# Performance work log

Measured on AMD Instinct MI355X. Metric: run time of the kernel, lower is better.

The kernel has to match this reference:

```python
import jax, jax.numpy as jnp
import numpy as np

B, C, H, W = 16, 3, 224, 224
P = 16
DIM = 256
NL = 8
DS = 16          # d_state (mamba default)
DCONV = 4
NCLS = 1000
DI = 2 * DIM     # expand * dim
DTR = -(-DIM // 16)  # dt_rank = ceil(dim/16)
NPATCH = (H // P) * (W // P)
SEQ = NPATCH + 1


def _ln(x, g, b, eps=1e-5):
    mu = x.mean(-1, keepdims=True)
    var = ((x - mu) ** 2).mean(-1, keepdims=True)
    return (x - mu) * jax.lax.rsqrt(var + eps) * g + b


def setup_inputs() -> dict:
    key = jax.random.key(0)
    ks = jax.random.split(key, 12)
    pd = C * P * P
    s = 0.02
    return dict(
        img=jax.random.normal(ks[0], (B, C, H, W), jnp.float32),
        pe_ln1_g=jnp.ones((pd,), jnp.float32), pe_ln1_b=jnp.zeros((pd,), jnp.float32),
        pe_w=jax.random.normal(ks[1], (pd, DIM), jnp.float32) * s,
        pe_b=jnp.zeros((DIM,), jnp.float32),
        pe_ln2_g=jnp.ones((DIM,), jnp.float32), pe_ln2_b=jnp.zeros((DIM,), jnp.float32),
        pos_emb=jax.random.normal(ks[2], (1, SEQ, DIM), jnp.float32) * s,
        cls_tok=jax.random.normal(ks[3], (1, 1, DIM), jnp.float32) * s,
        ln_w=jnp.ones((NL, DIM), jnp.float32), ln_b=jnp.zeros((NL, DIM), jnp.float32),
        in_w=jax.random.normal(ks[4], (NL, DIM, 2 * DI), jnp.float32) * s,
        conv_w=jax.random.normal(ks[5], (NL, DI, DCONV), jnp.float32) * s,
        conv_b=jnp.zeros((NL, DI), jnp.float32),
        xproj_w=jax.random.normal(ks[6], (NL, DI, DTR + 2 * DS), jnp.float32) * s,
        dtproj_w=jax.random.normal(ks[7], (NL, DTR, DI), jnp.float32) * s,
        dtproj_b=jax.random.uniform(ks[8], (NL, DI), jnp.float32, -4.0, -2.0),
        A_log=jnp.log(jnp.broadcast_to(jnp.arange(1, DS + 1, dtype=jnp.float32), (NL, DI, DS))) + jnp.zeros((NL, DI, DS), jnp.float32),
        Dp=jnp.ones((NL, DI), jnp.float32),
        out_w=jax.random.normal(ks[9], (NL, DI, DIM), jnp.float32) * s,
        normf_w=jnp.ones((DIM,), jnp.float32), normf_b=jnp.zeros((DIM,), jnp.float32),
        head_w=jax.random.normal(ks[10], (DIM, NCLS), jnp.float32) * s,
        head_b=jnp.zeros((NCLS,), jnp.float32),
    )


def _mamba(x, in_w, conv_w, conv_b, xproj_w, dtproj_w, dtproj_b, A_log, Dp, out_w):
    b, L, _ = x.shape
    xz = x @ in_w                       # (b, L, 2*DI)
    xm, z = jnp.split(xz, 2, axis=-1)
    # causal depthwise conv1d (torch pads both sides then slices -> left-pad d_conv-1)
    xc = jnp.pad(xm.transpose(0, 2, 1), ((0, 0), (0, 0), (DCONV - 1, 0)))
    xc = jax.lax.conv_general_dilated(
        xc, conv_w[:, None, :], (1,), 'VALID',
        dimension_numbers=('NCH', 'OIH', 'NCH'), feature_group_count=DI)
    u = jax.nn.silu(xc + conv_b[None, :, None]).transpose(0, 2, 1)  # (b, L, DI)
    dbc = u @ xproj_w                   # (b, L, DTR+2*DS)
    dt, Bm, Cm = jnp.split(dbc, [DTR, DTR + DS], axis=-1)
    dt = jax.nn.softplus(dt @ dtproj_w + dtproj_b)  # (b, L, DI)
    A = -jnp.exp(A_log)                 # (DI, DS)

    def step(h, inp):
        dt_t, B_t, C_t, u_t = inp       # (b,DI), (b,DS), (b,DS), (b,DI)
        dA = jnp.exp(dt_t[:, :, None] * A)                 # (b, DI, DS)
        h = dA * h + (dt_t * u_t)[:, :, None] * B_t[:, None, :]
        y = jnp.einsum('bdn,bn->bd', h, C_t)
        return h, y

    h0 = jnp.zeros((b, DI, DS), x.dtype)
    xs = (dt.transpose(1, 0, 2), Bm.transpose(1, 0, 2),
          Cm.transpose(1, 0, 2), u.transpose(1, 0, 2))
    _, ys = jax.lax.scan(step, h0, xs)
    y = ys.transpose(1, 0, 2) + u * Dp  # (b, L, DI)
    y = y * jax.nn.silu(z)
    return y @ out_w                    # (b, L, DIM)


def reference(img, pe_ln1_g, pe_ln1_b, pe_w, pe_b, pe_ln2_g, pe_ln2_b, pos_emb,
              cls_tok, ln_w, ln_b, in_w, conv_w, conv_b, xproj_w, dtproj_w,
              dtproj_b, A_log, Dp, out_w, normf_w, normf_b, head_w, head_b):
    b = img.shape[0]
    h, w = H // P, W // P
    # 'b c (h p1) (w p2) -> b (h w) (p1 p2 c)'
    x = img.reshape(b, C, h, P, w, P).transpose(0, 2, 4, 3, 5, 1).reshape(b, h * w, P * P * C)
    x = _ln(x, pe_ln1_g, pe_ln1_b)
    x = x @ pe_w + pe_b
    x = _ln(x, pe_ln2_g, pe_ln2_b)
    x = jnp.concatenate([jnp.broadcast_to(cls_tok, (b, 1, DIM)), x], axis=1)
    x = x + pos_emb[:, :x.shape[1]]
    residual = None
    for i in range(NL):
        residual = x if residual is None else x + residual
        xn = _ln(residual, ln_w[i], ln_b[i])
        x = _mamba(xn, in_w[i], conv_w[i], conv_b[i], xproj_w[i],
                   dtproj_w[i], dtproj_b[i], A_log[i], Dp[i], out_w[i])
    residual = x + residual
    x = _ln(residual, normf_w, normf_b)
    x = x[:, 0]                          # pool == 'cls'
    return x @ head_w + head_b
```

## Files before the change

### kernel.cpp

```cpp
#include <hip/hip_runtime.h>
#include <math.h>

#define NB   16
#define SEQL 197
#define TB   (NB*SEQL)
#define DIMM 256
#define DI   512
#define DS   16
#define NL   8

typedef __bf16 bf16x8 __attribute__((ext_vector_type(8)));
typedef __bf16 bf16x4 __attribute__((ext_vector_type(4)));
typedef float floatx4 __attribute__((ext_vector_type(4)));

__device__ __forceinline__ void block_reduce_2(float& s1, float& s2, float* red, int tid){
  #pragma unroll
  for (int off = 32; off > 0; off >>= 1){
    s1 += __shfl_down(s1, off, 64);
    s2 += __shfl_down(s2, off, 64);
  }
  __syncthreads();
  if ((tid & 63) == 0){ red[(tid>>6)*2] = s1; red[(tid>>6)*2+1] = s2; }
  __syncthreads();
  s1 = red[0] + red[2] + red[4] + red[6];
  s2 = red[1] + red[3] + red[5] + red[7];
}

__global__ __launch_bounds__(256) void prep_weights(
    const float* __restrict__ in_w, const float* __restrict__ out_w,
    const float* __restrict__ pe_w, const float* __restrict__ xproj,
    __bf16* __restrict__ wt_in, __bf16* __restrict__ wt_out,
    __bf16* __restrict__ wt_pe, __bf16* __restrict__ wt_xp)
{
  __shared__ float t[32][33];
  int bid = blockIdx.x;
  const float* src; __bf16* dst;
  int K, Nin, n0, k0;
  if (bid < 2048){
    int z = bid >> 8, tt = bid & 255;
    K = 256; Nin = 1024; n0 = (tt & 31)*32; k0 = (tt >> 5)*32;
    src = in_w  + (size_t)z*K*Nin;
    dst = wt_in + (size_t)z*K*Nin;
  } else if (bid < 3072){
    int t2 = bid - 2048; int z = t2 >> 7, tt = t2 & 127;
    K = 512; Nin = 256; n0 = (tt & 7)*32; k0 = (tt >> 3)*32;
    src = out_w  + (size_t)z*K*Nin;
    dst = wt_out + (size_t)z*K*Nin;
  } else if (bid < 3264){
    int tt = bid - 3072;
    K = 768; Nin = 256; n0 = (tt & 7)*32; k0 = (tt >> 3)*32;
    src = pe_w; dst = wt_pe;
  } else {
    int t2 = bid - 3264; int z = t2 >> 5, tt = t2 & 31;
    K = 512; Nin = 48; n0 = (tt & 1)*32; k0 = (tt >> 1)*32;
    src = xproj + (size_t)z*K*Nin;
    dst = wt_xp + (size_t)z*64*K;
  }
  int tx = threadIdx.x & 31, ty = threadIdx.x >> 5;
  #pragma unroll
  for (int j = 0; j < 4; j++){
    int n = n0 + tx;
    t[ty + j*8][tx] = (n < Nin) ? src[(size_t)(k0 + ty + j*8)*Nin + n] : 0.f;
  }
  __syncthreads();
  #pragma unroll
  for (int j = 0; j < 4; j++)
    dst[(size_t)(n0 + ty + j*8)*K + k0 + tx] = (__bf16)t[tx][ty + j*8];
}

template<int BM, int BN, int KS>
__global__ __launch_bounds__(256) void gemm_bf16(
    const __bf16* __restrict__ A, const __bf16* __restrict__ Wt,
    const float* __restrict__ bias, float* __restrict__ C, int M, int N, int K)
{
  constexpr int BK  = 32;
  constexpr int LDA = BK + 8;
  constexpr int TMW = BM/32;
  constexpr int TNW = BN/32;
  __shared__ __bf16 As[BM][LDA];
  __shared__ __bf16 Bs[BN][LDA];

  int tid  = threadIdx.x;
  int lane = tid & 63, w = tid >> 6;
  int wm = w >> 1, wn = w & 1;
  int l15 = lane & 15, quad = lane >> 4;
  int nt = blockIdx.x / KS, ks = blockIdx.x % KS;
  int bm = blockIdx.y * BM, bn = nt * BN;
  int kbeg = ks * (K / KS), kend = kbeg + (K / KS);

  floatx4 acc[TMW][TNW] = {};

  for (int k0 = kbeg; k0 < kend; k0 += BK){
    #pragma unroll
    for (int i = 0; i < BM/64; i++){
      int c = tid + i*256;
      int row = c >> 2, kc = c & 3;
      int m = bm + row;
      uint4 v = make_uint4(0,0,0,0);
      if (m < M) v = ((const uint4*)(A + (size_t)m*K + k0))[kc];
      *(uint4*)&As[row][kc*8] = v;
    }
    #pragma unroll
    for (int i = 0; i < BN/64; i++){
      int c = tid + i*256;
      int row = c >> 2, kc = c & 3;
      int n = bn + row;
      uint4 v = ((const uint4*)(Wt + (size_t)n*K + k0))[kc];
      *(uint4*)&Bs[row][kc*8] = v;
    }
    __syncthreads();
    bf16x8 af[TMW], bf[TNW];
    #pragma unroll
    for (int mi = 0; mi < TMW; mi++)
      af[mi] = *(const bf16x8*)&As[wm*(BM/2) + mi*16 + l15][quad*8];
    #pragma unroll
    for (int ni = 0; ni < TNW; ni++)
      bf[ni] = *(const bf16x8*)&Bs[wn*(BN/2) + ni*16 + l15][quad*8];
    #pragma unroll
    for (int mi = 0; mi < TMW; mi++)
      #pragma unroll
      for (int ni = 0; ni < TNW; ni++)
        acc[mi][ni] = __builtin_amdgcn_mfma_f32_16x16x32_bf16(af[mi], bf[ni], acc[mi][ni], 0, 0, 0);
    __syncthreads();
  }
  #pragma unroll
  for (int mi = 0; mi < TMW; mi++){
    #pragma unroll
    for (int ni = 0; ni < TNW; ni++){
      int col = bn + wn*(BN/2) + ni*16 + l15;
      float bv = (KS == 1 && bias) ? bias[col] : 0.f;
      #pragma unroll
      for (int r = 0; r < 4; r++){
        int row = bm + wm*(BM/2) + mi*16 + quad*4 + r;
        if (row < M){
          if (KS == 1) C[(size_t)row*N + col] = acc[mi][ni][r] + bv;
          else         atomicAdd(&C[(size_t)row*N + col], acc[mi][ni][r]);
        }
      }
    }
  }
}

template<int DO_LN>
__global__ __launch_bounds__(512) void gemm_out_fused(
    const __bf16* __restrict__ A, const __bf16* __restrict__ Wt,
    float* __restrict__ resid, __bf16* __restrict__ xn_bf,
    const float* __restrict__ g, const float* __restrict__ bta)
{
  constexpr int BK = 64, LDA = BK + 8;
  __shared__ alignas(16) char smem[(16 + 256) * LDA * sizeof(__bf16)];
  __bf16 (*As)[LDA] = (__bf16(*)[LDA])smem;
  __bf16 (*Bs)[LDA] = (__bf16(*)[LDA])(smem + 16*LDA*sizeof(__bf16));
  float  (*sy)[264] = (float(*)[264])smem;

  int tid = threadIdx.x, lane = tid & 63, w = tid >> 6;
  int l15 = lane & 15, quad = lane >> 4;
  int bm = blockIdx.x * 16;

  floatx4 acc[2] = {};
  for (int k0 = 0; k0 < 512; k0 += BK){
    if (tid < 128){
      int row = tid >> 3, kc = tid & 7;
      *(uint4*)&As[row][kc*8] = ((const uint4*)(A + (size_t)(bm+row)*512 + k0))[kc];
    }
    #pragma unroll
    for (int i = 0; i < 4; i++){
      int c = tid + i*512;
      int row = c >> 3, kc = c & 7;
      *(uint4*)&Bs[row][kc*8] = ((const uint4*)(Wt + (size_t)row*512 + k0))[kc];
    }
    __syncthreads();
    #pragma unroll
    for (int kk = 0; kk < 2; kk++){
      bf16x8 af = *(const bf16x8*)&As[l15][kk*32 + quad*8];
      #pragma unroll
      for (int ni = 0; ni < 2; ni++){
        bf16x8 bfv = *(const bf16x8*)&Bs[w*32 + ni*16 + l15][kk*32 + quad*8];
        acc[ni] = __builtin_amdgcn_mfma_f32_16x16x32_bf16(af, bfv, acc[ni], 0, 0, 0);
      }
    }
    __syncthreads();
  }
  #pragma unroll
  for (int ni = 0; ni < 2; ni++){
    int col = w*32 + ni*16 + l15;
    #pragma unroll
    for (int r = 0; r < 4; r++)
      sy[quad*4 + r][col] = acc[ni][r];
  }
  __syncthreads();
  #pragma unroll
  for (int rr = 0; rr < 2; rr++){
    int row = w*2 + rr;
    size_t base = (size_t)(bm + row)*256 + lane*4;
    float4 y4 = *(const float4*)&sy[row][lane*4];
    float4 rv = *(const float4*)&resid[base];
    float4 v;
    v.x = y4.x + rv.x; v.y = y4.y + rv.y; v.z = y4.z + rv.z; v.w = y4.w + rv.w;
    *(float4*)&resid[base] = v;
    if (DO_LN){
      float s  = v.x + v.y + v.z + v.w;
      float s2 = v.x*v.x + v.y*v.y + v.z*v.z + v.w*v.w;
      #pragma unroll
      for (int off = 1; off < 64; off <<= 1){
        s  += __shfl_xor(s,  off, 64);
        s2 += __shfl_xor(s2, off, 64);
      }
      float mu  = s * (1.f/256.f);
      float var = s2 * (1.f/256.f) - mu*mu;
      float rrq = rsqrtf(var + 1e-5f);
      float4 gv = *(const float4*)&g[lane*4];
      float4 bv = *(const float4*)&bta[lane*4];
      bf16x4 o;
      o[0] = (__bf16)((v.x - mu)*rrq*gv.x + bv.x);
      o[1] = (__bf16)((v.y - mu)*rrq*gv.y + bv.y);
      o[2] = (__bf16)((v.z - mu)*rrq*gv.z + bv.z);
      o[3] = (__bf16)((v.w - mu)*rrq*gv.w + bv.w);
      *(bf16x4*)&xn_bf[base] = o;
    }
  }
}

__global__ __launch_bounds__(256) void patch_ln1(
    const float* __restrict__ img, const float* __restrict__ g1, const float* __restrict__ b1,
    __bf16* __restrict__ xp_bf)
{
  __shared__ float red[8];
  int blk = blockIdx.x;
  int b = blk / 196, p = blk % 196;
  int hh = p / 14, ww = p % 14;
  int tid = threadIdx.x;

  float v[3]; float s = 0.f, s2 = 0.f;
  #pragma unroll
  for (int i = 0; i < 3; i++){
    int e  = tid + i*256;
    int c  = e % 3;
    int p2 = (e/3) % 16;
    int p1 = e / 48;
    float val = img[((b*3 + c)*224 + hh*16 + p1)*224 + ww*16 + p2];
    v[i] = val; s += val; s2 += val*val;
  }
  block_reduce_2(s, s2, red, tid);
  float mu = s * (1.f/768.f);
  float var = s2 * (1.f/768.f) - mu*mu;
  float rr = rsqrtf(var + 1e-5f);
  #pragma unroll
  for (int i = 0; i < 3; i++){
    int e = tid + i*256;
    xp_bf[(size_t)blk*768 + e] = (__bf16)((v[i] - mu) * rr * g1[e] + b1[e]);
  }
}

__global__ __launch_bounds__(256) void ln2_cls_pos(
    const float* __restrict__ pemb, const float* __restrict__ g2, const float* __restrict__ b2,
    const float* __restrict__ pos, const float* __restrict__ cls,
    float* __restrict__ resid,
    const float* __restrict__ g0, const float* __restrict__ b0,
    __bf16* __restrict__ xn_bf)
{
  __shared__ float red[8];
  int blk = blockIdx.x;
  int b = blk / SEQL, l = blk % SEQL;
  int tid = threadIdx.x;
  float o;
  if (l == 0){
    o = cls[tid] + pos[tid];
  } else {
    int p = l - 1;
    float v = pemb[(size_t)(b*196 + p)*256 + tid];
    float s = v, s2 = v*v;
    block_reduce_2(s, s2, red, tid);
    float mu = s * (1.f/256.f);
    float var = s2 * (1.f/256.f) - mu*mu;
    float rr = rsqrtf(var + 1e-5f);
    o = (v - mu) * rr * g2[tid] + b2[tid] + pos[l*256 + tid];
  }
  size_t idx = (size_t)blk*256 + tid;
  resid[idx] = o;
  float s = o, s2 = o*o;
  block_reduce_2(s, s2, red, tid);
  float mu = s * (1.f/256.f);
  float var = s2 * (1.f/256.f) - mu*mu;
  float rr = rsqrtf(var + 1e-5f);
  xn_bf[idx] = (__bf16)((o - mu) * rr * g0[tid] + b0[tid]);
}

__global__ __launch_bounds__(256) void conv_silu(
    const float* __restrict__ xz, const float* __restrict__ cw, const float* __restrict__ cb,
    float* __restrict__ u, __bf16* __restrict__ u_bf, float* __restrict__ dbc)
{
  int gid = blockIdx.x*256 + threadIdx.x;
  int dq = gid & 127;
  int t = gid >> 7;
  int d = dq*4;
  int l = t % SEQL;
  const float4 z4 = make_float4(0.f,0.f,0.f,0.f);
  if (dq < 16) *(float4*)&dbc[(size_t)t*64 + d] = z4;
  float4 x0 = *(const float4*)&xz[(size_t)t*1024 + d];
  float4 x1 = (l>=1) ? *(const float4*)&xz[(size_t)(t-1)*1024 + d] : z4;
  float4 x2 = (l>=2) ? *(const float4*)&xz[(size_t)(t-2)*1024 + d] : z4;
  float4 x3 = (l>=3) ? *(const float4*)&xz[(size_t)(t-3)*1024 + d] : z4;
  float4 w0 = *(const float4*)&cw[(d+0)*4];
  float4 w1 = *(const float4*)&cw[(d+1)*4];
  float4 w2 = *(const float4*)&cw[(d+2)*4];
  float4 w3 = *(const float4*)&cw[(d+3)*4];
  float4 r = *(const float4*)&cb[d];
  r.x += x3.x*w0.x + x2.x*w0.y + x1.x*w0.z + x0.x*w0.w;
  r.y += x3.y*w1.x + x2.y*w1.y + x1.y*w1.z + x0.y*w1.w;
  r.z += x3.z*w2.x + x2.z*w2.y + x1.z*w2.z + x0.z*w2.w;
  r.w += x3.w*w3.x + x2.w*w3.y + x1.w*w3.z + x0.w*w3.w;
  r.x *= 1.f/(1.f + __expf(-r.x));
  r.y *= 1.f/(1.f + __expf(-r.y));
  r.z *= 1.f/(1.f + __expf(-r.z));
  r.w *= 1.f/(1.f + __expf(-r.w));
  *(float4*)&u[(size_t)t*512 + d] = r;
  bf16x4 o; o[0]=(__bf16)r.x; o[1]=(__bf16)r.y; o[2]=(__bf16)r.z; o[3]=(__bf16)r.w;
  *(bf16x4*)&u_bf[(size_t)t*512 + d] = o;
}

#define SCT 32
#define NCH ((SEQL + SCT - 1)/SCT)
#define NDL 8
__global__ __launch_bounds__(128) void scan_kernel(
    const float* __restrict__ u, const float* __restrict__ dbc,
    const float* __restrict__ xz, const float* __restrict__ A_log, const float* __restrict__ Dp,
    const float* __restrict__ dtw, const float* __restrict__ dtb,
    __bf16* __restrict__ yg_bf)
{
  __shared__ float s_D [16][36];
  __shared__ float s_B [16][36];
  __shared__ float s_C [16][36];
  __shared__ float s_u [NDL][36];
  __shared__ float s_z [NDL][36];
  __shared__ float s_dt[NDL][36];
  __shared__ float s_yp[SCT][NDL][20];
  __shared__ float s_dp[NDL];

  int tid = threadIdx.x;
  int n = tid & 15, dl = tid >> 4;
  int b = blockIdx.x >> 6, dg = blockIdx.x & 63;
  int d0 = dg * NDL;
  const size_t base = (size_t)b * SEQL;

  float A = -__expf(A_log[(d0+dl)*DS + n]);
  float h = 0.f;
  if (tid < NDL) s_dp[tid] = Dp[d0 + tid];
  int cch = tid & 7;
  float wc[16];
  #pragma unroll
  for (int k = 0; k < 16; k++) wc[k] = dtw[k*512 + d0 + cch];
  float dtbv = dtb[d0 + cch];

  float r_u[2], r_z[2], r_db[12];
  auto load_regs = [&](int c){
    #pragma unroll
    for (int i = 0; i < 2; i++){
      int v = tid + i*128;
      int tg = c*SCT + (v>>3); if (tg > SEQL-1) tg = SEQL-1;
      size_t t = base + tg;
      r_u[i] = u [t*512 + d0 + (v&7)];
      r_z[i] = xz[t*1024 + 512 + d0 + (v&7)];
    }
    #pragma unroll
    for (int s = 0; s < 3; s++)
      #pragma unroll
      for (int i = 0; i < 4; i++){
        int v = tid + i*128;
        int tg = c*SCT + (v>>4); if (tg > SEQL-1) tg = SEQL-1;
        r_db[s*4+i] = dbc[(base + tg)*64 + s*16 + (v&15)];
      }
  };
  auto write_DBC = [&](){
    #pragma unroll
    for (int i = 0; i < 4; i++){
      int v = tid + i*128;
      s_D[v&15][v>>4] = r_db[0+i];
      s_B[v&15][v>>4] = r_db[4+i];
      s_C[v&15][v>>4] = r_db[8+i];
    }
  };
  auto write_UZ = [&](){
    #pragma unroll
    for (int i = 0; i < 2; i++){
      int v = tid + i*128;
      s_u[v&7][v>>3] = r_u[i];
      s_z[v&7][v>>3] = r_z[i];
    }
  };
  auto compute_dt = [&](){
    #pragma unroll
    for (int i = 0; i < 2; i++){
      int tl = (tid >> 3) + i*16;
      float acc = dtbv;
      #pragma unroll
      for (int k = 0; k < 16; k++) acc += s_D[k][tl] * wc[k];
      s_dt[cch][tl] = (acc > 20.f) ? acc : log1pf(__expf(acc));
    }
  };

  load_regs(0);
  write_DBC();
  write_UZ();
  __syncthreads();
  compute_dt();
  __syncthreads();

  for (int c = 0; c < NCH; c++){
    if (c + 1 < NCH) load_regs(c+1);

    float4 dt4, u4, B4, C4;
    #pragma unroll
    for (int tl = 0; tl < SCT; tl++){
      if ((tl & 3) == 0){
        dt4 = *(const float4*)&s_dt[dl][tl];
        u4  = *(const float4*)&s_u [dl][tl];
        B4  = *(const float4*)&s_B [n][tl];
        C4  = *(const float4*)&s_C [n][tl];
      }
      float dtv = ((float*)&dt4)[tl&3];
      float uv  = ((float*)&u4 )[tl&3];
      float Bv  = ((float*)&B4 )[tl&3];
      float Cv  = ((float*)&C4 )[tl&3];
      h = __expf(dtv * A) * h + (dtv * uv) * Bv;
      s_yp[tl][dl][n] = h * Cv;
    }
    __syncthreads();

    if (c + 1 < NCH) write_DBC();

    #pragma unroll
    for (int j = 0; j < 2; j++){
      int p = tid + j*128;
      int tl = p >> 3, dr = p & 7;
      float4 a0 = *(const float4*)&s_yp[tl][dr][0];
      float4 a1 = *(const float4*)&s_yp[tl][dr][4];
      float4 a2 = *(const float4*)&s_yp[tl][dr][8];
      float4 a3 = *(const float4*)&s_yp[tl][dr][12];
      float yv = ((a0.x+a0.y)+(a0.z+a0.w)) + ((a1.x+a1.y)+(a1.z+a1.w))
               + ((a2.x+a2.y)+(a2.z+a2.w)) + ((a3.x+a3.y)+(a3.z+a3.w));
      int tg = c*SCT + tl;
      if (tg < SEQL){
        float uv = s_u[dr][tl];
        float zv = s_z[dr][tl];
        float sg = 1.f / (1.f + __expf(-zv));
        yg_bf[(base + tg)*512 + d0 + dr] = (__bf16)((yv + uv*s_dp[dr]) * zv * sg);
      }
    }
    __syncthreads();

    if (c + 1 < NCH){
      write_UZ();
      compute_dt();
      __syncthreads();
    }
  }
}

__global__ __launch_bounds__(256) void final_ln(
    const float* __restrict__ resid,
    const float* __restrict__ g, const float* __restrict__ bta, float* __restrict__ xs_g)
{
  __shared__ float red[8];
  int b = blockIdx.x, tid = threadIdx.x;
  size_t idx = (size_t)b*SEQL*256 + tid;
  float r = resid[idx];
  float s = r, s2 = r*r;
  block_reduce_2(s, s2, red, tid);
  float mu = s * (1.f/256.f);
  float var = s2 * (1.f/256.f) - mu*mu;
  float rr = rsqrtf(var + 1e-5f);
  xs_g[b*256 + tid] = (r - mu) * rr * g[tid] + bta[tid];
}

__global__ __launch_bounds__(256) void head_gemm(
    const float* __restrict__ xs_g, const float* __restrict__ head_w,
    const float* __restrict__ head_b, float* __restrict__ out)
{
  __shared__ float xs[16][256];
  int tid = threadIdx.x;
  #pragma unroll
  for (int i = 0; i < 16; i++) ((float*)xs)[tid + i*256] = xs_g[tid + i*256];
  __syncthreads();
  int nl = tid & 31, bq = tid >> 5;
  int nn = blockIdx.x*32 + nl;
  if (nn >= 1000) return;
  float acc0 = 0.f, acc1 = 0.f;
  #pragma unroll 8
  for (int k = 0; k < 256; k++){
    float w = head_w[k*1000 + nn];
    acc0 += xs[bq][k]   * w;
    acc1 += xs[bq+8][k] * w;
  }
  float hb = head_b[nn];
  out[(size_t)bq*1000 + nn]     = acc0 + hb;
  out[(size_t)(bq+8)*1000 + nn] = acc1 + hb;
}

extern "C" void kernel_launch(void* const* d_in, const int* in_sizes, int n_in,
                              void* d_out, int out_size, void* d_ws, size_t ws_size,
                              hipStream_t stream) {
  const float* img   = (const float*)d_in[0];
  const float* ln1g  = (const float*)d_in[1];
  const float* ln1b  = (const float*)d_in[2];
  const float* pe_w  = (const float*)d_in[3];
  const float* pe_b  = (const float*)d_in[4];
  const float* ln2g  = (const float*)d_in[5];
  const float* ln2b  = (const float*)d_in[6];
  const float* pos   = (const float*)d_in[7];
  const float* cls   = (const float*)d_in[8];
  const float* ln_w  = (const float*)d_in[9];
  const float* ln_b  = (const float*)d_in[10];
  const float* in_w  = (const float*)d_in[11];
  const float* conv_w= (const float*)d_in[12];
  const float* conv_b= (const float*)d_in[13];
  const float* xproj = (const float*)d_in[14];
  const float* dtw   = (const float*)d_in[15];
  const float* dtb   = (const float*)d_in[16];
  const float* A_log = (const float*)d_in[17];
  const float* Dp    = (const float*)d_in[18];
  const float* out_w = (const float*)d_in[19];
  const float* nfw   = (const float*)d_in[20];
  const float* nfb   = (const float*)d_in[21];
  const float* head_w= (const float*)d_in[22];
  const float* head_b= (const float*)d_in[23];
  float* out = (float*)d_out;

  float* ws = (float*)d_ws;
  float* resid = ws;  ws += (size_t)TB*DIMM;
  float* xz    = ws;  ws += (size_t)TB*2*DI;
  float* u     = ws;  ws += (size_t)TB*DI;
  float* dbc   = ws;  ws += (size_t)TB*64;
  float* xs_g  = ws;  ws += (size_t)NB*DIMM;
  __bf16* xn_bf = (__bf16*)ws;  ws += (size_t)TB*DIMM/2;
  __bf16* u_bf  = (__bf16*)ws;  ws += (size_t)TB*DI/2;
  __bf16* yg_bf = (__bf16*)ws;  ws += (size_t)TB*DI/2;
  __bf16* wt_in = (__bf16*)ws;  ws += (size_t)NL*1024*256/2;
  __bf16* wt_out= (__bf16*)ws;  ws += (size_t)NL*256*512/2;
  __bf16* wt_pe = (__bf16*)ws;  ws += (size_t)256*768/2;
  __bf16* wt_xp = (__bf16*)ws;  ws += (size_t)NL*64*512/2;
  __bf16* xp_bf = (__bf16*)xz;
  float*  pemb  = u;

  prep_weights<<<3520, 256, 0, stream>>>(in_w, out_w, pe_w, xproj,
                                          wt_in, wt_out, wt_pe, wt_xp);

  patch_ln1<<<NB*196, 256, 0, stream>>>(img, ln1g, ln1b, xp_bf);
  gemm_bf16<64,64,1><<<dim3(256/64, 3136/64), 256, 0, stream>>>(
      xp_bf, wt_pe, pe_b, pemb, 3136, 256, 768);
  ln2_cls_pos<<<NB*SEQL, 256, 0, stream>>>(pemb, ln2g, ln2b, pos, cls,
                                           resid, ln_w, ln_b, xn_bf);

  for (int i = 0; i < NL; i++){
    gemm_bf16<64,128,1><<<dim3(1024/128, (TB+63)/64), 256, 0, stream>>>(
        xn_bf, wt_in + (size_t)i*1024*256, nullptr, xz, TB, 1024, 256);
    conv_silu<<<TB*128/256, 256, 0, stream>>>(
        xz, conv_w + i*DI*4, conv_b + i*DI, u, u_bf, dbc);
    gemm_bf16<64,64,4><<<dim3(4, (TB+63)/64), 256, 0, stream>>>(
        u_bf, wt_xp + (size_t)i*64*512, nullptr, dbc, TB, 64, 512);
    scan_kernel<<<NB*64, 128, 0, stream>>>(
        u, dbc, xz, A_log + i*DI*DS, Dp + i*DI, dtw + i*16*DI, dtb + i*DI, yg_bf);
    if (i < NL-1)
      gemm_out_fused<1><<<TB/16, 512, 0, stream>>>(
          yg_bf, wt_out + (size_t)i*256*512, resid, xn_bf,
          ln_w + (i+1)*DIMM, ln_b + (i+1)*DIMM);
    else
      gemm_out_fused<0><<<TB/16, 512, 0, stream>>>(
          yg_bf, wt_out + (size_t)i*256*512, resid, nullptr, nullptr, nullptr);
  }
  final_ln<<<NB, 256, 0, stream>>>(resid, nfw, nfb, xs_g);
  head_gemm<<<(1000+31)/32, 256, 0, stream>>>(xs_g, head_w, head_b, out);
}
```

Baseline: 659.1 us.

## Fuse depthwise conv+SiLU with x_proj GEMM into one fp32 kernel

Replaces the conv_silu kernel and the separate bf16 x_proj GEMM (split-K with atomic accumulation into a zeroed dbc) with a single kernel. Each block computes conv+SiLU for 4 tokens into shared memory, then does the 512x48 projection in fp32 from a transposed fp32 weight copy. This removes one launch per layer, the u_bf write and re-read, and the dbc zeroing and atomics. In exchange the projection runs on plain FMA instead of MFMA, and each block re-reads the 128KB weight slice for only 4 tokens.

```diff
diff --git a/kernel.cpp b/kernel.cpp
--- a/kernel.cpp
+++ b/kernel.cpp
@@ -30,11 +30,11 @@
     const float* __restrict__ in_w, const float* __restrict__ out_w,
     const float* __restrict__ pe_w, const float* __restrict__ xproj,
     __bf16* __restrict__ wt_in, __bf16* __restrict__ wt_out,
-    __bf16* __restrict__ wt_pe, __bf16* __restrict__ wt_xp)
+    __bf16* __restrict__ wt_pe, float* __restrict__ wt_xp_f)
 {
   __shared__ float t[32][33];
   int bid = blockIdx.x;
-  const float* src; __bf16* dst;
+  const float* src; __bf16* dst = nullptr; float* dstf = nullptr;
   int K, Nin, n0, k0;
   if (bid < 2048){
     int z = bid >> 8, tt = bid & 255;
@@ -53,8 +53,8 @@
   } else {
     int t2 = bid - 3264; int z = t2 >> 5, tt = t2 & 31;
     K = 512; Nin = 48; n0 = (tt & 1)*32; k0 = (tt >> 1)*32;
-    src = xproj + (size_t)z*K*Nin;
-    dst = wt_xp + (size_t)z*64*K;
+    src  = xproj + (size_t)z*K*Nin;
+    dstf = wt_xp_f + (size_t)z*64*512;
   }
   int tx = threadIdx.x & 31, ty = threadIdx.x >> 5;
   #pragma unroll
@@ -63,9 +63,15 @@
     t[ty + j*8][tx] = (n < Nin) ? src[(size_t)(k0 + ty + j*8)*Nin + n] : 0.f;
   }
   __syncthreads();
-  #pragma unroll
-  for (int j = 0; j < 4; j++)
-    dst[(size_t)(n0 + ty + j*8)*K + k0 + tx] = (__bf16)t[tx][ty + j*8];
+  if (dstf){
+    #pragma unroll
+    for (int j = 0; j < 4; j++)
+      dstf[(size_t)(n0 + ty + j*8)*K + k0 + tx] = t[tx][ty + j*8];
+  } else {
+    #pragma unroll
+    for (int j = 0; j < 4; j++)
+      dst[(size_t)(n0 + ty + j*8)*K + k0 + tx] = (__bf16)t[tx][ty + j*8];
+  }
 }
 
 template<int BM, int BN, int KS>
@@ -286,37 +292,76 @@
   xn_bf[idx] = (__bf16)((o - mu) * rr * g0[tid] + b0[tid]);
 }
 
-__global__ __launch_bounds__(256) void conv_silu(
+__global__ __launch_bounds__(256) void conv_xproj(
     const float* __restrict__ xz, const float* __restrict__ cw, const float* __restrict__ cb,
-    float* __restrict__ u, __bf16* __restrict__ u_bf, float* __restrict__ dbc)
-{
-  int gid = blockIdx.x*256 + threadIdx.x;
-  int dq = gid & 127;
-  int t = gid >> 7;
-  int d = dq*4;
-  int l = t % SEQL;
-  const float4 z4 = make_float4(0.f,0.f,0.f,0.f);
-  if (dq < 16) *(float4*)&dbc[(size_t)t*64 + d] = z4;
-  float4 x0 = *(const float4*)&xz[(size_t)t*1024 + d];
-  float4 x1 = (l>=1) ? *(const float4*)&xz[(size_t)(t-1)*1024 + d] : z4;
-  float4 x2 = (l>=2) ? *(const float4*)&xz[(size_t)(t-2)*1024 + d] : z4;
-  float4 x3 = (l>=3) ? *(const float4*)&xz[(size_t)(t-3)*1024 + d] : z4;
+    const float* __restrict__ wxp,
+    float* __restrict__ u, float* __restrict__ dbc)
+{
+  __shared__ float s_u[4][512];
+  __shared__ float s_acc[4][4][64];
+  int tid = threadIdx.x;
+  int t0 = blockIdx.x * 4;
+
+  int d = (tid & 127) * 4;
   float4 w0 = *(const float4*)&cw[(d+0)*4];
   float4 w1 = *(const float4*)&cw[(d+1)*4];
   float4 w2 = *(const float4*)&cw[(d+2)*4];
   float4 w3 = *(const float4*)&cw[(d+3)*4];
-  float4 r = *(const float4*)&cb[d];
-  r.x += x3.x*w0.x + x2.x*w0.y + x1.x*w0.z + x0.x*w0.w;
-  r.y += x3.y*w1.x + x2.y*w1.y + x1.y*w1.z + x0.y*w1.w;
-  r.z += x3.z*w2.x + x2.z*w2.y + x1.z*w2.z + x0.z*w2.w;
-  r.w += x3.w*w3.x + x2.w*w3.y + x1.w*w3.z + x0.w*w3.w;
-  r.x *= 1.f/(1.f + __expf(-r.x));
-  r.y *= 1.f/(1.f + __expf(-r.y));
-  r.z *= 1.f/(1.f + __expf(-r.z));
-  r.w *= 1.f/(1.f + __expf(-r.w));
-  *(float4*)&u[(size_t)t*512 + d] = r;
-  bf16x4 o; o[0]=(__bf16)r.x; o[1]=(__bf16)r.y; o[2]=(__bf16)r.z; o[3]=(__bf16)r.w;
-  *(bf16x4*)&u_bf[(size_t)t*512 + d] = o;
+  float4 cbv = *(const float4*)&cb[d];
+  const float4 z4 = make_float4(0.f,0.f,0.f,0.f);
+  #pragma unroll
+  for (int j = 0; j < 2; j++){
+    int tl = (tid >> 7)*2 + j;
+    int t = t0 + tl;
+    int l = t % SEQL;
+    float4 x0 = *(const float4*)&xz[(size_t)t*1024 + d];
+    float4 x1 = (l>=1) ? *(const float4*)&xz[(size_t)(t-1)*1024 + d] : z4;
+    float4 x2 = (l>=2) ? *(const float4*)&xz[(size_t)(t-2)*1024 + d] : z4;
+    float4 x3 = (l>=3) ? *(const float4*)&xz[(size_t)(t-3)*1024 + d] : z4;
+    float4 r = cbv;
+    r.x += x3.x*w0.x + x2.x*w0.y + x1.x*w0.z + x0.x*w0.w;
+    r.y += x3.y*w1.x + x2.y*w1.y + x1.y*w1.z + x0.y*w1.w;
+    r.z += x3.z*w2.x + x2.z*w2.y + x1.z*w2.z + x0.z*w2.w;
+    r.w += x3.w*w3.x + x2.w*w3.y + x1.w*w3.z + x0.w*w3.w;
+    r.x *= 1.f/(1.f + __expf(-r.x));
+    r.y *= 1.f/(1.f + __expf(-r.y));
+    r.z *= 1.f/(1.f + __expf(-r.z));
+    r.w *= 1.f/(1.f + __expf(-r.w));
+    *(float4*)&u[(size_t)t*512 + d] = r;
+    *(float4*)&s_u[tl][d] = r;
+  }
+  __syncthreads();
+
+  int col = tid & 63, sl = tid >> 6;
+  const float* wp = wxp + (size_t)col*512 + sl*128;
+  const float* u0p = &s_u[0][sl*128];
+  const float* u1p = &s_u[1][sl*128];
+  const float* u2p = &s_u[2][sl*128];
+  const float* u3p = &s_u[3][sl*128];
+  float a0 = 0.f, a1 = 0.f, a2 = 0.f, a3 = 0.f;
+  #pragma unroll 8
+  for (int kk = 0; kk < 128; kk += 4){
+    float4 wv = *(const float4*)&wp[kk];
+    float4 v0 = *(const float4*)&u0p[kk];
+    float4 v1 = *(const float4*)&u1p[kk];
+    float4 v2 = *(const float4*)&u2p[kk];
+    float4 v3 = *(const float4*)&u3p[kk];
+    a0 += wv.x*v0.x + wv.y*v0.y + wv.z*v0.z + wv.w*v0.w;
+    a1 += wv.x*v1.x + wv.y*v1.y + wv.z*v1.z + wv.w*v1.w;
+    a2 += wv.x*v2.x + wv.y*v2.y + wv.z*v2.z + wv.w*v2.w;
+    a3 += wv.x*v3.x + wv.y*v3.y + wv.z*v3.z + wv.w*v3.w;
+  }
+  s_acc[sl][0][col] = a0;
+  s_acc[sl][1][col] = a1;
+  s_acc[sl][2][col] = a2;
+  s_acc[sl][3][col] = a3;
+  __syncthreads();
+  int tok = tid >> 6, c2 = tid & 63;
+  if (c2 < 48){
+    float v = s_acc[0][tok][c2] + s_acc[1][tok][c2]
+            + s_acc[2][tok][c2] + s_acc[3][tok][c2];
+    dbc[(size_t)(t0 + tok)*64 + c2] = v;
+  }
 }
 
 #define SCT 32
@@ -532,18 +577,17 @@
   float* u     = ws;  ws += (size_t)TB*DI;
   float* dbc   = ws;  ws += (size_t)TB*64;
   float* xs_g  = ws;  ws += (size_t)NB*DIMM;
+  float* wt_xp_f = ws; ws += (size_t)NL*64*512;
   __bf16* xn_bf = (__bf16*)ws;  ws += (size_t)TB*DIMM/2;
-  __bf16* u_bf  = (__bf16*)ws;  ws += (size_t)TB*DI/2;
   __bf16* yg_bf = (__bf16*)ws;  ws += (size_t)TB*DI/2;
   __bf16* wt_in = (__bf16*)ws;  ws += (size_t)NL*1024*256/2;
   __bf16* wt_out= (__bf16*)ws;  ws += (size_t)NL*256*512/2;
   __bf16* wt_pe = (__bf16*)ws;  ws += (size_t)256*768/2;
-  __bf16* wt_xp = (__bf16*)ws;  ws += (size_t)NL*64*512/2;
   __bf16* xp_bf = (__bf16*)xz;
   float*  pemb  = u;
 
   prep_weights<<<3520, 256, 0, stream>>>(in_w, out_w, pe_w, xproj,
-                                          wt_in, wt_out, wt_pe, wt_xp);
+                                          wt_in, wt_out, wt_pe, wt_xp_f);
 
   patch_ln1<<<NB*196, 256, 0, stream>>>(img, ln1g, ln1b, xp_bf);
   gemm_bf16<64,64,1><<<dim3(256/64, 3136/64), 256, 0, stream>>>(
@@ -554,10 +598,8 @@
   for (int i = 0; i < NL; i++){
     gemm_bf16<64,128,1><<<dim3(1024/128, (TB+63)/64), 256, 0, stream>>>(
         xn_bf, wt_in + (size_t)i*1024*256, nullptr, xz, TB, 1024, 256);
-    conv_silu<<<TB*128/256, 256, 0, stream>>>(
-        xz, conv_w + i*DI*4, conv_b + i*DI, u, u_bf, dbc);
-    gemm_bf16<64,64,4><<<dim3(4, (TB+63)/64), 256, 0, stream>>>(
-        u_bf, wt_xp + (size_t)i*64*512, nullptr, dbc, TB, 64, 512);
+    conv_xproj<<<TB/4, 256, 0, stream>>>(
+        xz, conv_w + i*DI*4, conv_b + i*DI, wt_xp_f + (size_t)i*64*512, u, dbc);
     scan_kernel<<<NB*64, 128, 0, stream>>>(
         u, dbc, xz, A_log + i*DI*DS, Dp + i*DI, dtw + i*16*DI, dtb + i*DI, yg_bf);
     if (i < NL-1)
```

After: 726.9 us. 10.3% more time.
